# Performance work log

Hardware: AMD Instinct MI355X
Metric: run time of the kernel (lower is better)

The kernel has to match this reference:

```python
import jax, jax.numpy as jnp
import numpy as np

E, D, H, B, S = 16, 1024, 256, 4, 4096  # num_splats, model_dim, ff_dim//num_splats, batch, seq_len


def setup_inputs() -> dict:
    key = jax.random.key(0)
    ks = jax.random.split(key, 8)
    s = 0.02  # init scale for stability
    return {
        "x": jax.random.normal(ks[0], (B, S, D), dtype=jnp.float32),
        "splat_id": jax.random.randint(ks[1], (S,), 0, E, dtype=jnp.int32),
        "W1": jax.random.normal(ks[2], (E, D, H), dtype=jnp.float32) * s,
        "b1": jnp.zeros((E, H), dtype=jnp.float32),
        "W2": jax.random.normal(ks[3], (E, H, D), dtype=jnp.float32) * s,
        "b2": jnp.zeros((E, D), dtype=jnp.float32),
        "Wg1": jax.random.normal(ks[4], (D, D), dtype=jnp.float32) * s,
        "bg1": jnp.zeros((D,), dtype=jnp.float32),
        "Wg2": jax.random.normal(ks[5], (D, D), dtype=jnp.float32) * s,
        "bg2": jnp.zeros((D,), dtype=jnp.float32),
    }


def reference(x, splat_id, W1, b1, W2, b2, Wg1, bg1, Wg2, bg2):
    # Splat-aware dispatch: token s is processed by expert splat_id[s].
    # Equivalent vectorized form: run every expert's small MLP, mask at the
    # hidden layer by expert assignment, and sum over experts (each token is
    # assigned to exactly one expert, matching the gather->MLP->scatter loop).
    nE = W1.shape[0]
    onehot = (splat_id[None, :] == jnp.arange(nE, dtype=splat_id.dtype)[:, None]).astype(x.dtype)  # [E,S]
    # hidden: [E,B,S,H]
    h = jax.nn.gelu(jnp.einsum('bsd,edh->ebsh', x, W1) + b1[:, None, None, :], approximate=False)
    h = h * onehot[:, None, :, None]  # zero tokens not routed to expert e
    routed = jnp.einsum('ebsh,ehd->bsd', h, W2)  # [B,S,D]
    routed = routed + jnp.einsum('es,ed->sd', onehot, b2)[None, :, :]  # per-token expert bias
    # global aggregator MLP (torch GELU default = exact erf form)
    g = jax.nn.gelu(routed @ Wg1 + bg1, approximate=False)
    return g @ Wg2 + bg2
```

## Files before the change

kernel.cpp:

```cpp
#include <hip/hip_runtime.h>


#define DEV __device__ __forceinline__

typedef float f32x4 __attribute__((ext_vector_type(4)));
typedef short short8 __attribute__((ext_vector_type(8)));

DEV unsigned short f2bf(float f) {
  unsigned u = __float_as_uint(f);
  u += 0x7fffu + ((u >> 16) & 1u);
  return (unsigned short)(u >> 16);
}

DEV void gload16(const void* g, void* l) {
  __builtin_amdgcn_global_load_lds(
      (const __attribute__((address_space(1))) unsigned int*)g,
      (__attribute__((address_space(3))) unsigned int*)l, 16, 0, 0);
}

DEV float gelu_exact(float v) {
  return 0.5f * v * (1.0f + erff(v * 0.70710678118654752f));
}

#define BARRIER() __builtin_amdgcn_s_barrier()
#define VMW(n)    asm volatile("s_waitcnt vmcnt(" #n ")" ::: "memory")

__global__ __launch_bounds__(256) void prep_kernel(
    const float* __restrict__ W1, unsigned short* __restrict__ w1t,
    const float* __restrict__ W2, unsigned short* __restrict__ w2t,
    const float* __restrict__ Wg1, unsigned short* __restrict__ wg1t,
    const float* __restrict__ Wg2, unsigned short* __restrict__ wg2t) {
  __shared__ float tile[64][65];
  const int t = threadIdx.x;
  int id = (int)blockIdx.x;
  const float* in; unsigned short* out;
  int R, C, r0, c0; long base;
  if (id < 1024) {
    in = W1; out = w1t; R = 1024; C = 256;
    base = (long)(id >> 6) * 262144;
    r0 = ((id >> 2) & 15) * 64; c0 = (id & 3) * 64;
  } else if (id < 2048) {
    id -= 1024;
    in = W2; out = w2t; R = 256; C = 1024;
    base = (long)(id >> 6) * 262144;
    r0 = ((id >> 4) & 3) * 64; c0 = (id & 15) * 64;
  } else if (id < 2304) {
    id -= 2048;
    in = Wg1; out = wg1t; R = 1024; C = 1024; base = 0;
    r0 = (id >> 4) * 64; c0 = (id & 15) * 64;
  } else {
    id -= 2304;
    in = Wg2; out = wg2t; R = 1024; C = 1024; base = 0;
    r0 = (id >> 4) * 64; c0 = (id & 15) * 64;
  }
  const int cc = t & 63, rr = t >> 6;
#pragma unroll
  for (int i = 0; i < 16; i++) {
    int r = rr + i * 4;
    tile[r][cc] = in[base + (long)(r0 + r) * C + (c0 + cc)];
  }
  __syncthreads();
#pragma unroll
  for (int i = 0; i < 16; i++) {
    int c = rr + i * 4;
    out[base + (long)(c0 + c) * R + (r0 + cc)] = f2bf(tile[cc][c]);
  }
}

__global__ __launch_bounds__(256) void route_kernel(
    const int* __restrict__ sid, int S, int* __restrict__ offs, int* __restrict__ order,
    int* __restrict__ tileE, int* __restrict__ tileR, int* __restrict__ ntl) {
  __shared__ int cnt[16], cur[16];
  const int t = threadIdx.x;
  if (t < 16) cnt[t] = 0;
  __syncthreads();
  for (int s = t; s < S; s += 256) atomicAdd(&cnt[sid[s]], 1);
  __syncthreads();
  if (t == 0) {
    int a = 0;
    for (int e = 0; e < 16; e++) { offs[e] = a; cur[e] = a; a += cnt[e]; }
    offs[16] = a;
    int nt = 0;
    for (int e = 0; e < 16; e++) {
      const int rows = 4 * cnt[e];
      for (int r = 0; r < rows; r += 64) {
        tileE[nt] = e;
        tileR[nt] = 4 * offs[e] + r;
        nt++;
      }
    }
    ntl[0] = nt;
  }
  __syncthreads();
  for (int s = t; s < S; s += 256) {
    int p = atomicAdd(&cur[sid[s]], 1);
    order[p] = s;
  }
}

__global__ __launch_bounds__(512, 2) void fused_expert(
    const float* __restrict__ x,
    const unsigned short* __restrict__ w1t, const float* __restrict__ b1,
    const unsigned short* __restrict__ w2t, const float* __restrict__ b2,
    unsigned short* __restrict__ rout,
    const int* __restrict__ order, const int* __restrict__ offs,
    const int* __restrict__ tileE, const int* __restrict__ tileR,
    const int* __restrict__ ntl) {
  constexpr int S = 4096, D = 1024, H = 256;
  const int ti = (int)blockIdx.x;
  if (ti >= ntl[0]) return;

  __shared__ __align__(16) unsigned short lA[64 * 64];
  __shared__ __align__(16) unsigned short lB[256 * 64];
  __shared__ __align__(16) unsigned short hS[64 * 256];

  const int t = (int)threadIdx.x;
  const int lane = t & 63;
  const int w = t >> 6;
  const int wm = w >> 2;
  const int wn = w & 3;

  const int e = tileE[ti];
  const int rowBase = tileR[ti];
  int Me = 4 * offs[e + 1] - rowBase;
  if (Me > 64) Me = 64;

  const int ar = t >> 3;
  const int arr = (ar < Me) ? ar : (Me - 1);
  const int ga = rowBase + arr;
  const float* xsrc = x + ((long)(ga & 3) * S + order[ga >> 2]) * D + (t & 7) * 8;
  unsigned short* aDst = lA + ar * 64 + (((((t & 7) * 16)) ^ ((ar & 7) << 4)) >> 1);

  const unsigned short* b1src[4];
#pragma unroll
  for (int i = 0; i < 4; i++) {
    const int row = i * 64 + (t >> 3);
    b1src[i] = w1t + (long)e * H * D + (long)row * D + ((((t & 7) * 16) ^ ((row & 7) << 4)) >> 1);
  }
  const int dstE = (t >> 3) * 64 + (t & 7) * 8;

  f32x4 acc[2][4] = {};
  float4 xv0 = *(const float4*)(xsrc);
  float4 xv1 = *(const float4*)(xsrc + 4);

  for (int kt = 0; kt < 16; kt++) {
    __syncthreads();
    short8 av;
    av[0] = (short)f2bf(xv0.x); av[1] = (short)f2bf(xv0.y);
    av[2] = (short)f2bf(xv0.z); av[3] = (short)f2bf(xv0.w);
    av[4] = (short)f2bf(xv1.x); av[5] = (short)f2bf(xv1.y);
    av[6] = (short)f2bf(xv1.z); av[7] = (short)f2bf(xv1.w);
    *(short8*)aDst = av;
#pragma unroll
    for (int i = 0; i < 4; i++) gload16(b1src[i] + (kt << 6), lB + i * 4096 + dstE);
    if (kt < 15) {
      xv0 = *(const float4*)(xsrc + (kt + 1) * 64);
      xv1 = *(const float4*)(xsrc + (kt + 1) * 64 + 4);
    }
    __syncthreads();
#pragma unroll
    for (int kk = 0; kk < 2; kk++) {
      short8 aF[2], bF[4];
      const int kb = kk * 64 + ((lane >> 4) << 4);
#pragma unroll
      for (int mi = 0; mi < 2; mi++) {
        const int row = wm * 32 + mi * 16 + (lane & 15);
        aF[mi] = *(const short8*)((const char*)lA + row * 128 + (kb ^ ((row & 7) << 4)));
      }
#pragma unroll
      for (int ni = 0; ni < 4; ni++) {
        const int row = wn * 64 + ni * 16 + (lane & 15);
        bF[ni] = *(const short8*)((const char*)lB + row * 128 + (kb ^ ((row & 7) << 4)));
      }
#pragma unroll
      for (int mi = 0; mi < 2; mi++)
#pragma unroll
        for (int ni = 0; ni < 4; ni++)
          acc[mi][ni] = __builtin_amdgcn_mfma_f32_16x16x32_bf16(aF[mi], bF[ni], acc[mi][ni], 0, 0, 0);
    }
  }

  {
    float bc[4];
#pragma unroll
    for (int ni = 0; ni < 4; ni++)
      bc[ni] = b1[e * H + wn * 64 + ni * 16 + (lane & 15)];
#pragma unroll
    for (int mi = 0; mi < 2; mi++)
#pragma unroll
      for (int j = 0; j < 4; j++) {
        const int crow = wm * 32 + mi * 16 + ((lane >> 4) << 2) + j;
#pragma unroll
        for (int ni = 0; ni < 4; ni++) {
          const int ccol = wn * 64 + ni * 16 + (lane & 15);
          const float v = gelu_exact(acc[mi][ni][j] + bc[ni]);
          hS[crow * 256 + (((ccol * 2) ^ ((crow & 7) << 4)) >> 1)] = f2bf(v);
        }
      }
  }
  __syncthreads();

  const unsigned short* b2base = w2t + (long)e * D * H;
  for (int nc = 0; nc < 8; nc++) {
    f32x4 a2[2][2] = {};
    for (int ks = 0; ks < 4; ks++) {
      __syncthreads();
#pragma unroll
      for (int i = 0; i < 2; i++) {
        const int row = i * 64 + (t >> 3);
        const unsigned short* src = b2base + (long)(nc * 128 + row) * H + (ks << 6) +
                                    ((((t & 7) * 16) ^ ((row & 7) << 4)) >> 1);
        gload16(src, lB + i * 4096 + dstE);
      }
      __syncthreads();
#pragma unroll
      for (int kk = 0; kk < 2; kk++) {
        short8 aF[2], bF[2];
        const int kbh = ks * 128 + kk * 64 + ((lane >> 4) << 4);
        const int kb = kk * 64 + ((lane >> 4) << 4);
#pragma unroll
        for (int mi = 0; mi < 2; mi++) {
          const int row = wm * 32 + mi * 16 + (lane & 15);
          aF[mi] = *(const short8*)((const char*)hS + row * 512 + (kbh ^ ((row & 7) << 4)));
        }
#pragma unroll
        for (int ni = 0; ni < 2; ni++) {
          const int row = wn * 32 + ni * 16 + (lane & 15);
          bF[ni] = *(const short8*)((const char*)lB + row * 128 + (kb ^ ((row & 7) << 4)));
        }
#pragma unroll
        for (int mi = 0; mi < 2; mi++)
#pragma unroll
          for (int ni = 0; ni < 2; ni++)
            a2[mi][ni] = __builtin_amdgcn_mfma_f32_16x16x32_bf16(aF[mi], bF[ni], a2[mi][ni], 0, 0, 0);
      }
    }
    float bc2[2];
#pragma unroll
    for (int ni = 0; ni < 2; ni++)
      bc2[ni] = b2[e * D + nc * 128 + wn * 32 + ni * 16 + (lane & 15)];
#pragma unroll
    for (int mi = 0; mi < 2; mi++)
#pragma unroll
      for (int j = 0; j < 4; j++) {
        const int lrow = wm * 32 + mi * 16 + ((lane >> 4) << 2) + j;
        if (lrow >= Me) continue;
        const int g = rowBase + lrow;
        const long crow = (long)(g & 3) * S + order[g >> 2];
#pragma unroll
        for (int ni = 0; ni < 2; ni++) {
          const float v = a2[mi][ni][j] + bc2[ni];
          rout[crow * D + nc * 128 + wn * 32 + ni * 16 + (lane & 15)] = f2bf(v);
        }
      }
  }
}

template <bool GELU, bool OUT_F32>
__global__ __launch_bounds__(512, 1) void gemm_2ph(
    const unsigned short* __restrict__ A, const unsigned short* __restrict__ BT,
    const float* __restrict__ bias, void* __restrict__ Cout,
    int N, int K, int ntiles) {
  __shared__ __align__(16) unsigned short lds[2][2][256 * 64];

  const int t = (int)threadIdx.x;
  const int lane = t & 63;
  const int w = t >> 6;
  const int wm = w >> 2;
  const int wn = w & 3;

  const int cpx = (int)gridDim.x >> 3;
  const int swz = ((int)blockIdx.x & 7) * cpx + ((int)blockIdx.x >> 3);
  const int mtile = swz / ntiles, ntile = swz % ntiles;

  const int tq = t & 7;
  const unsigned short* srcA[4];
  const unsigned short* srcB[4];
#pragma unroll
  for (int i = 0; i < 4; i++) {
    const int row = i * 64 + (t >> 3);
    const int koffE = ((tq * 16) ^ ((row & 7) << 4)) >> 1;
    srcA[i] = A + (long)(mtile * 256 + row) * K + koffE;
    srcB[i] = BT + (long)(ntile * 256 + row) * K + koffE;
  }
  const int dstE = (t >> 3) * 64 + tq * 8;

  auto STAGE = [&](int buf, int kt) {
    const long ko = (long)kt << 6;
#pragma unroll
    for (int i = 0; i < 4; i++) gload16(srcA[i] + ko, &lds[buf][0][i * 4096 + dstE]);
#pragma unroll
    for (int i = 0; i < 4; i++) gload16(srcB[i] + ko, &lds[buf][1][i * 4096 + dstE]);
  };

  f32x4 acc[8][4] = {};
  const int KT = K >> 6;

  STAGE(0, 0);
  __syncthreads();

  int buf = 0;
  for (int kt = 0; kt < KT; kt++) {
    if (kt + 1 < KT) STAGE(buf ^ 1, kt + 1);
#pragma unroll
    for (int kk = 0; kk < 2; kk++) {
      short8 aF[8], bF[4];
      const int kb = kk * 64 + ((lane >> 4) << 4);
#pragma unroll
      for (int m = 0; m < 8; m++) {
        const int row = wm * 128 + m * 16 + (lane & 15);
        aF[m] = *(const short8*)((const char*)&lds[buf][0][0] + row * 128 + (kb ^ ((row & 7) << 4)));
      }
#pragma unroll
      for (int n = 0; n < 4; n++) {
        const int row = wn * 64 + n * 16 + (lane & 15);
        bF[n] = *(const short8*)((const char*)&lds[buf][1][0] + row * 128 + (kb ^ ((row & 7) << 4)));
      }
      __builtin_amdgcn_s_setprio(1);
#pragma unroll
      for (int m = 0; m < 8; m++)
#pragma unroll
        for (int n = 0; n < 4; n++)
          acc[m][n] = __builtin_amdgcn_mfma_f32_16x16x32_bf16(aF[m], bF[n], acc[m][n], 0, 0, 0);
      __builtin_amdgcn_s_setprio(0);
    }
    __syncthreads();
    buf ^= 1;
  }

  float bcol[4];
#pragma unroll
  for (int n = 0; n < 4; n++)
    bcol[n] = bias[ntile * 256 + wn * 64 + n * 16 + (lane & 15)];
  const int cbase = ntile * 256 + wn * 64 + (lane & 15);
#pragma unroll
  for (int m = 0; m < 8; m++) {
#pragma unroll
    for (int j = 0; j < 4; j++) {
      const long crow = mtile * 256 + wm * 128 + m * 16 + ((lane >> 4) << 2) + j;
#pragma unroll
      for (int n = 0; n < 4; n++) {
        float v = acc[m][n][j] + bcol[n];
        if (GELU) v = gelu_exact(v);
        const long cidx = crow * (long)N + cbase + n * 16;
        if (OUT_F32) ((float*)Cout)[cidx] = v;
        else ((unsigned short*)Cout)[cidx] = f2bf(v);
      }
    }
  }
}

template <bool GELU, bool OUT_F32>
__global__ __launch_bounds__(512, 2) void gemm_8phase(
    const unsigned short* __restrict__ A, const unsigned short* __restrict__ BT,
    const float* __restrict__ bias, void* __restrict__ Cout,
    int N, int K, int ntiles) {
  __shared__ __align__(16) unsigned short lds[8 * 8192];

  const int t = (int)threadIdx.x;
  const int lane = t & 63;
  const int w = t >> 6;
  const int wm = w >> 2;
  const int wn = w & 3;

  const int cpx = (int)gridDim.x >> 3;
  const int swz = ((int)blockIdx.x & 7) * cpx + ((int)blockIdx.x >> 3);
  const int mtile = swz / ntiles, ntile = swz % ntiles;

  const int tq = t & 7;
  const unsigned short* srcA[2][2];
  const unsigned short* srcB[2][2];
#pragma unroll
  for (int i = 0; i < 2; i++) {
    const int ir = i * 64 + (t >> 3);
    const int koffE = ((tq * 16) ^ ((ir & 7) << 4)) >> 1;
#pragma unroll
    for (int h = 0; h < 2; h++) {
      const int ra = (ir & 63) + (h << 6) + ((ir >> 6) << 7);
      srcA[i][h] = A + (long)(mtile * 256 + ra) * K + koffE;
      const int cb = (ir & 31) + (h << 5) + ((ir >> 5) << 6);
      srcB[i][h] = BT + (long)(ntile * 256 + cb) * K + koffE;
    }
  }
  const int dstE = (t >> 3) * 64 + tq * 8;

  auto STAGE = [&](int d, int mat, int h, int kt) {
    unsigned short* dst = lds + ((d * 4 + mat * 2 + h) << 13) + dstE;
    const unsigned short* s0 = (mat == 0 ? srcA[0][h] : srcB[0][h]) + (kt << 6);
    const unsigned short* s1 = (mat == 0 ? srcA[1][h] : srcB[1][h]) + (kt << 6);
    gload16(s0, dst);
    gload16(s1, dst + 4096);
  };

  short8 aReg[8], bReg[8];
  const int klane = (lane >> 4) << 4;
  const int rsw = (lane & 7) << 4;

  auto LDA = [&](int d, int mh) {
    const char* base = (const char*)(lds + ((d * 4 + mh) << 13));
    const int r0 = wm * 64 + (lane & 15);
#pragma unroll
    for (int m = 0; m < 4; m++) {
      const int row = r0 + m * 16;
#pragma unroll
      for (int kk = 0; kk < 2; kk++)
        aReg[m * 2 + kk] = *(const short8*)(base + row * 128 + ((kk * 64 + klane) ^ rsw));
    }
  };
  auto LDB = [&](int d, int nh) {
    const char* base = (const char*)(lds + ((d * 4 + 2 + nh) << 13));
    const int r0 = wn * 32 + (lane & 15);
#pragma unroll
    for (int n = 0; n < 2; n++) {
      const int row = r0 + n * 16;
#pragma unroll
      for (int kk = 0; kk < 2; kk++)
        bReg[(nh * 2 + n) * 2 + kk] = *(const short8*)(base + row * 128 + ((kk * 64 + klane) ^ rsw));
    }
  };

  f32x4 acc[8][4] = {};
  auto MMA = [&](int mb, int nb) {
    __builtin_amdgcn_s_setprio(1);
#pragma unroll
    for (int kk = 0; kk < 2; kk++)
#pragma unroll
      for (int m = 0; m < 4; m++)
#pragma unroll
        for (int n = 0; n < 2; n++)
          acc[mb + m][nb + n] = __builtin_amdgcn_mfma_f32_16x16x32_bf16(
              aReg[m * 2 + kk], bReg[(nb + n) * 2 + kk], acc[mb + m][nb + n], 0, 0, 0);
    __builtin_amdgcn_s_setprio(0);
  };

  const int KT = K >> 6;

  {
    const int t1 = (KT > 1) ? 1 : 0;
    STAGE(0, 0, 0, 0); STAGE(0, 1, 0, 0); STAGE(0, 1, 1, 0); STAGE(0, 0, 1, 0);
    STAGE(1, 0, 0, t1); STAGE(1, 1, 0, t1); STAGE(1, 1, 1, t1);
    VMW(6);
    BARRIER();
  }

  for (int it = 0; it < (KT >> 1); ++it) {
    const int tb = (2 * it + 1 < KT) ? 2 * it + 1 : KT - 1;
    int nx = 2 * it + 2; if (nx >= KT) nx = KT - 1;
    int ny = 2 * it + 3; if (ny >= KT) ny = KT - 1;
    LDA(0, 0); LDB(0, 0); STAGE(1, 0, 1, tb);
    BARRIER();
    MMA(0, 0);
    BARRIER();
    LDB(0, 1); STAGE(0, 0, 0, nx);
    BARRIER();
    MMA(0, 2);
    BARRIER();
    LDA(0, 1); STAGE(0, 1, 0, nx);
    BARRIER();
    MMA(4, 0);
    BARRIER();
    STAGE(0, 1, 1, nx);
    BARRIER();
    MMA(4, 2);
    VMW(6);
    BARRIER();
    LDA(1, 0); LDB(1, 0); STAGE(0, 0, 1, nx);
    BARRIER();
    MMA(0, 0);
    BARRIER();
    LDB(1, 1); STAGE(1, 0, 0, ny);
    BARRIER();
    MMA(0, 2);
    BARRIER();
    LDA(1, 1); STAGE(1, 1, 0, ny);
    BARRIER();
    MMA(4, 0);
    BARRIER();
    STAGE(1, 1, 1, ny);
    BARRIER();
    MMA(4, 2);
    VMW(6);
    BARRIER();
  }
  VMW(0);

  float bcol[4];
#pragma unroll
  for (int n = 0; n < 4; n++)
    bcol[n] = bias[ntile * 256 + wn * 64 + n * 16 + (lane & 15)];
  const int cbase = ntile * 256 + wn * 64 + (lane & 15);
#pragma unroll
  for (int m = 0; m < 8; m++) {
#pragma unroll
    for (int j = 0; j < 4; j++) {
      const long crow = mtile * 256 + wm * 128 + m * 16 + ((lane >> 4) << 2) + j;
#pragma unroll
      for (int n = 0; n < 4; n++) {
        float v = acc[m][n][j] + bcol[n];
        if (GELU) v = gelu_exact(v);
        const long cidx = crow * (long)N + cbase + n * 16;
        if (OUT_F32) ((float*)Cout)[cidx] = v;
        else ((unsigned short*)Cout)[cidx] = f2bf(v);
      }
    }
  }
}

extern "C" void kernel_launch(void* const* d_in, const int* in_sizes, int n_in,
                              void* d_out, int out_size, void* d_ws, size_t ws_size,
                              hipStream_t stream) {
  const float* x   = (const float*)d_in[0];
  const int*   sid = (const int*)d_in[1];
  const float* W1  = (const float*)d_in[2];
  const float* b1  = (const float*)d_in[3];
  const float* W2  = (const float*)d_in[4];
  const float* b2  = (const float*)d_in[5];
  const float* Wg1 = (const float*)d_in[6];
  const float* bg1 = (const float*)d_in[7];
  const float* Wg2 = (const float*)d_in[8];
  const float* bg2 = (const float*)d_in[9];
  (void)in_sizes; (void)n_in; (void)out_size; (void)ws_size;

  constexpr int D = 1024, S = 4096, B = 4;
  constexpr long NT = (long)B * S;

  char* ws = (char*)d_ws;
  unsigned short* g    = (unsigned short*)(ws);
  unsigned short* w1t  = (unsigned short*)(ws + 33554432);
  unsigned short* w2t  = (unsigned short*)(ws + 41943040);
  unsigned short* wg1t = (unsigned short*)(ws + 50331648);
  unsigned short* wg2t = (unsigned short*)(ws + 52428800);
  unsigned short* rout = (unsigned short*)(ws + 62914560);
  int* offs  = (int*)(ws + 96468992);
  int* order = (int*)(ws + 96469248);
  int* tileE = (int*)(ws + 96485632);
  int* tileR = (int*)(ws + 96486912);
  int* ntl   = (int*)(ws + 96488192);

  prep_kernel<<<dim3(2560), 256, 0, stream>>>(W1, w1t, W2, w2t, Wg1, wg1t, Wg2, wg2t);
  route_kernel<<<1, 256, 0, stream>>>(sid, S, offs, order, tileE, tileR, ntl);

  fused_expert<<<dim3(272), 512, 0, stream>>>(
      x, w1t, b1, w2t, b2, rout, order, offs, tileE, tileR, ntl);

  gemm_2ph<true, false><<<dim3((unsigned)(NT / 256) * (D / 256)), 512, 0, stream>>>(
      rout, wg1t, bg1, g, D, D, D / 256);
  gemm_8phase<false, true><<<dim3((unsigned)(NT / 256) * (D / 256)), 512, 0, stream>>>(
      g, wg2t, bg2, d_out, D, D, D / 256);
}
```

Before: 182.0 us.

## Double-buffer LDS tiles in fused expert kernel to overlap loads with MFMA

```diff
diff --git a/kernel.cpp b/kernel.cpp
--- a/kernel.cpp
+++ b/kernel.cpp
@@ -98,7 +98,7 @@
   }
 }
 
-__global__ __launch_bounds__(512, 2) void fused_expert(
+__global__ __launch_bounds__(512, 1) void fused_expert(
     const float* __restrict__ x,
     const unsigned short* __restrict__ w1t, const float* __restrict__ b1,
     const unsigned short* __restrict__ w2t, const float* __restrict__ b2,
@@ -110,8 +110,8 @@
   const int ti = (int)blockIdx.x;
   if (ti >= ntl[0]) return;
 
-  __shared__ __align__(16) unsigned short lA[64 * 64];
-  __shared__ __align__(16) unsigned short lB[256 * 64];
+  __shared__ __align__(16) unsigned short lA[2][64 * 64];
+  __shared__ __align__(16) unsigned short lB[2][256 * 64];
   __shared__ __align__(16) unsigned short hS[64 * 256];
 
   const int t = (int)threadIdx.x;
@@ -129,7 +129,7 @@
   const int arr = (ar < Me) ? ar : (Me - 1);
   const int ga = rowBase + arr;
   const float* xsrc = x + ((long)(ga & 3) * S + order[ga >> 2]) * D + (t & 7) * 8;
-  unsigned short* aDst = lA + ar * 64 + (((((t & 7) * 16)) ^ ((ar & 7) << 4)) >> 1);
+  const int aOff = ar * 64 + (((((t & 7) * 16)) ^ ((ar & 7) << 4)) >> 1);
 
   const unsigned short* b1src[4];
 #pragma unroll
@@ -139,25 +139,40 @@
   }
   const int dstE = (t >> 3) * 64 + (t & 7) * 8;
 
-  f32x4 acc[2][4] = {};
   float4 xv0 = *(const float4*)(xsrc);
   float4 xv1 = *(const float4*)(xsrc + 4);
 
-  for (int kt = 0; kt < 16; kt++) {
-    __syncthreads();
+  auto WLA = [&](int b) {
     short8 av;
     av[0] = (short)f2bf(xv0.x); av[1] = (short)f2bf(xv0.y);
     av[2] = (short)f2bf(xv0.z); av[3] = (short)f2bf(xv0.w);
     av[4] = (short)f2bf(xv1.x); av[5] = (short)f2bf(xv1.y);
     av[6] = (short)f2bf(xv1.z); av[7] = (short)f2bf(xv1.w);
-    *(short8*)aDst = av;
-#pragma unroll
-    for (int i = 0; i < 4; i++) gload16(b1src[i] + (kt << 6), lB + i * 4096 + dstE);
+    *(short8*)(&lA[b][0] + aOff) = av;
+  };
+  auto STAGE_B1 = [&](int b, int kt) {
+#pragma unroll
+    for (int i = 0; i < 4; i++) gload16(b1src[i] + (kt << 6), &lB[b][0] + i * 4096 + dstE);
+  };
+
+  f32x4 acc[2][4] = {};
+
+  WLA(0);
+  STAGE_B1(0, 0);
+  xv0 = *(const float4*)(xsrc + 64);
+  xv1 = *(const float4*)(xsrc + 64 + 4);
+  __syncthreads();
+
+  for (int kt = 0; kt < 16; kt++) {
+    const int cur = kt & 1, nxt = cur ^ 1;
     if (kt < 15) {
-      xv0 = *(const float4*)(xsrc + (kt + 1) * 64);
-      xv1 = *(const float4*)(xsrc + (kt + 1) * 64 + 4);
-    }
-    __syncthreads();
+      WLA(nxt);
+      STAGE_B1(nxt, kt + 1);
+      if (kt < 14) {
+        xv0 = *(const float4*)(xsrc + (kt + 2) * 64);
+        xv1 = *(const float4*)(xsrc + (kt + 2) * 64 + 4);
+      }
+    }
 #pragma unroll
     for (int kk = 0; kk < 2; kk++) {
       short8 aF[2], bF[4];
@@ -165,12 +180,12 @@
 #pragma unroll
       for (int mi = 0; mi < 2; mi++) {
         const int row = wm * 32 + mi * 16 + (lane & 15);
-        aF[mi] = *(const short8*)((const char*)lA + row * 128 + (kb ^ ((row & 7) << 4)));
+        aF[mi] = *(const short8*)((const char*)&lA[cur][0] + row * 128 + (kb ^ ((row & 7) << 4)));
       }
 #pragma unroll
       for (int ni = 0; ni < 4; ni++) {
         const int row = wn * 64 + ni * 16 + (lane & 15);
-        bF[ni] = *(const short8*)((const char*)lB + row * 128 + (kb ^ ((row & 7) << 4)));
+        bF[ni] = *(const short8*)((const char*)&lB[cur][0] + row * 128 + (kb ^ ((row & 7) << 4)));
       }
 #pragma unroll
       for (int mi = 0; mi < 2; mi++)
@@ -178,6 +193,7 @@
         for (int ni = 0; ni < 4; ni++)
           acc[mi][ni] = __builtin_amdgcn_mfma_f32_16x16x32_bf16(aF[mi], bF[ni], acc[mi][ni], 0, 0, 0);
     }
+    __syncthreads();
   }
 
   {
@@ -198,61 +214,75 @@
         }
       }
   }
-  __syncthreads();
 
   const unsigned short* b2base = w2t + (long)e * D * H;
-  for (int nc = 0; nc < 8; nc++) {
-    f32x4 a2[2][2] = {};
-    for (int ks = 0; ks < 4; ks++) {
-      __syncthreads();
-#pragma unroll
-      for (int i = 0; i < 2; i++) {
-        const int row = i * 64 + (t >> 3);
-        const unsigned short* src = b2base + (long)(nc * 128 + row) * H + (ks << 6) +
-                                    ((((t & 7) * 16) ^ ((row & 7) << 4)) >> 1);
-        gload16(src, lB + i * 4096 + dstE);
-      }
-      __syncthreads();
-#pragma unroll
-      for (int kk = 0; kk < 2; kk++) {
-        short8 aF[2], bF[2];
-        const int kbh = ks * 128 + kk * 64 + ((lane >> 4) << 4);
-        const int kb = kk * 64 + ((lane >> 4) << 4);
-#pragma unroll
-        for (int mi = 0; mi < 2; mi++) {
-          const int row = wm * 32 + mi * 16 + (lane & 15);
-          aF[mi] = *(const short8*)((const char*)hS + row * 512 + (kbh ^ ((row & 7) << 4)));
+  auto STAGE_W2 = [&](int b, int s) {
+    const int nc = s >> 2, ks = s & 3;
+#pragma unroll
+    for (int i = 0; i < 2; i++) {
+      const int row = i * 64 + (t >> 3);
+      const unsigned short* src = b2base + (long)(nc * 128 + row) * H + (ks << 6) +
+                                  ((((t & 7) * 16) ^ ((row & 7) << 4)) >> 1);
+      gload16(src, &lB[b][0] + i * 4096 + dstE);
+    }
+  };
+
+  STAGE_W2(0, 0);
+  __syncthreads();
+
+  f32x4 a2[2][2];
+  for (int s = 0; s < 32; s++) {
+    const int cur = s & 1, nxt = cur ^ 1;
+    const int nc = s >> 2, ks = s & 3;
+    if (s < 31) STAGE_W2(nxt, s + 1);
+    if (ks == 0) {
+#pragma unroll
+      for (int mi = 0; mi < 2; mi++)
+#pragma unroll
+        for (int ni = 0; ni < 2; ni++) a2[mi][ni] = (f32x4){0.f, 0.f, 0.f, 0.f};
+    }
+#pragma unroll
+    for (int kk = 0; kk < 2; kk++) {
+      short8 aF[2], bF[2];
+      const int kbh = ks * 128 + kk * 64 + ((lane >> 4) << 4);
+      const int kb = kk * 64 + ((lane >> 4) << 4);
+#pragma unroll
+      for (int mi = 0; mi < 2; mi++) {
+        const int row = wm * 32 + mi * 16 + (lane & 15);
+        aF[mi] = *(const short8*)((const char*)hS + row * 512 + (kbh ^ ((row & 7) << 4)));
+      }
+#pragma unroll
+      for (int ni = 0; ni < 2; ni++) {
+        const int row = wn * 32 + ni * 16 + (lane & 15);
+        bF[ni] = *(const short8*)((const char*)&lB[cur][0] + row * 128 + (kb ^ ((row & 7) << 4)));
+      }
+#pragma unroll
+      for (int mi = 0; mi < 2; mi++)
+#pragma unroll
+        for (int ni = 0; ni < 2; ni++)
+          a2[mi][ni] = __builtin_amdgcn_mfma_f32_16x16x32_bf16(aF[mi], bF[ni], a2[mi][ni], 0, 0, 0);
+    }
+    if (ks == 3) {
+      float bc2[2];
+#pragma unroll
+      for (int ni = 0; ni < 2; ni++)
+        bc2[ni] = b2[e * D + nc * 128 + wn * 32 + ni * 16 + (lane & 15)];
+#pragma unroll
+      for (int mi = 0; mi < 2; mi++)
+#pragma unroll
+        for (int j = 0; j < 4; j++) {
+          const int lrow = wm * 32 + mi * 16 + ((lane >> 4) << 2) + j;
+          if (lrow >= Me) continue;
+          const int g = rowBase + lrow;
+          const long crow = (long)(g & 3) * S + order[g >> 2];
+#pragma unroll
+          for (int ni = 0; ni < 2; ni++) {
+            const float v = a2[mi][ni][j] + bc2[ni];
+            rout[crow * D + nc * 128 + wn * 32 + ni * 16 + (lane & 15)] = f2bf(v);
+          }
         }
-#pragma unroll
-        for (int ni = 0; ni < 2; ni++) {
-          const int row = wn * 32 + ni * 16 + (lane & 15);
-          bF[ni] = *(const short8*)((const char*)lB + row * 128 + (kb ^ ((row & 7) << 4)));
-        }
-#pragma unroll
-        for (int mi = 0; mi < 2; mi++)
-#pragma unroll
-          for (int ni = 0; ni < 2; ni++)
-            a2[mi][ni] = __builtin_amdgcn_mfma_f32_16x16x32_bf16(aF[mi], bF[ni], a2[mi][ni], 0, 0, 0);
-      }
-    }
-    float bc2[2];
-#pragma unroll
-    for (int ni = 0; ni < 2; ni++)
-      bc2[ni] = b2[e * D + nc * 128 + wn * 32 + ni * 16 + (lane & 15)];
-#pragma unroll
-    for (int mi = 0; mi < 2; mi++)
-#pragma unroll
-      for (int j = 0; j < 4; j++) {
-        const int lrow = wm * 32 + mi * 16 + ((lane >> 4) << 2) + j;
-        if (lrow >= Me) continue;
-        const int g = rowBase + lrow;
-        const long crow = (long)(g & 3) * S + order[g >> 2];
-#pragma unroll
-        for (int ni = 0; ni < 2; ni++) {
-          const float v = a2[mi][ni][j] + bc2[ni];
-          rout[crow * D + nc * 128 + wn * 32 + ni * 16 + (lane & 15)] = f2bf(v);
-        }
-      }
+    }
+    __syncthreads();
   }
 }
 
```

New measurement: 223.8 us. 23.0% more time.
